# Kernel optimization log

Measured on AMD Instinct MI355X. Metric: run time of the kernel, lower is better.

## Reference

```python
import jax, jax.numpy as jnp
import numpy as np

TOPIC_K = 128
DOC_NUM = 500000
N_ONE = 2048
N_TWO = 64
EPS = 1e-12


def _l2norm(x, axis=-1):
    n = jnp.linalg.norm(x, axis=axis, keepdims=True)
    return x / jnp.maximum(n, EPS)


def _gnn_conv(v_feature, neighbor_mean, Wc, bc, Ws):
    # Conv: linear(neighbor_mean) + self_conv(v_feature) -> relu -> l2 normalize
    h = v_feature @ Ws.T + (neighbor_mean @ Wc.T + bc)
    return _l2norm(jax.nn.relu(h), axis=-1)


def setup_inputs() -> dict:
    key = jax.random.key(0)
    ks = jax.random.split(key, 12)
    K = TOPIC_K
    # Embedding table (xavier-uniform-ish scale)
    lim = float(np.sqrt(6.0 / (DOC_NUM + K)))
    emb = jax.random.uniform(ks[0], (DOC_NUM, K), jnp.float32, -lim, lim)
    s = 1.0 / np.sqrt(K)
    inp = {
        "emb": emb,
        # two_hop_conv params
        "Wc2h": jax.random.uniform(ks[1], (K, K), jnp.float32, -s, s),
        "bc2h": jax.random.uniform(ks[2], (K,), jnp.float32, -s, s),
        "Ws2h": jax.random.uniform(ks[3], (K, K), jnp.float32, -s, s),
        # one_hop_conv params
        "Wc1h": jax.random.uniform(ks[4], (K, K), jnp.float32, -s, s),
        "bc1h": jax.random.uniform(ks[5], (K,), jnp.float32, -s, s),
        "Ws1h": jax.random.uniform(ks[6], (K, K), jnp.float32, -s, s),
        # attention 1x1 single-channel conv weights == scalars
        "w_d": jax.random.normal(ks[7], (), jnp.float32),
        "w_W": jax.random.normal(ks[8], (), jnp.float32),
        "W_mat": jax.random.normal(ks[9], (1, K, K), jnp.float32),
        "v": jax.random.randint(ks[10], (1,), 0, DOC_NUM),
        "one_hop_list": jax.random.randint(ks[11], (N_ONE,), 0, DOC_NUM),
        "two_hop_list": jax.random.randint(jax.random.fold_in(key, 99), (N_ONE, N_TWO), 0, DOC_NUM),
    }
    return inp


def reference(emb, Wc2h, bc2h, Ws2h, Wc1h, bc1h, Ws1h, w_d, w_W, W_mat, v, one_hop_list, two_hop_list):
    # x: embedding of the ego vertex v[0]
    x = emb[v[0]]                                  # [K]
    one_feats = emb[one_hop_list]                  # [n_one, K]
    two_feats = emb[two_hop_list]                  # [n_one, n_two, K]
    # two-hop conv per one-hop neighbor (vectorized over n_one)
    two_mean = two_feats.mean(axis=1)              # [n_one, K]
    one_hop_features = _gnn_conv(one_feats, two_mean, Wc2h, bc2h, Ws2h)  # [n_one, K]
    # one-hop conv for ego vertex
    one_mean = one_hop_features.mean(axis=0)       # [K]
    x = _gnn_conv(x, one_mean, Wc1h, bc1h, Ws1h)   # [K]
    # Attention: 1x1 single-channel convs are scalar multiplies
    d = w_d * x                                    # [K]
    W = w_W * W_mat                                # [1, K, K]
    dW_T = jnp.einsum('k,bjk->bj', d, W)           # matmul(d, W.transpose(1,2)) -> [1, K]
    att = jax.nn.softmax(dW_T[:, None, :] * W_mat, axis=1)  # [1, K, K]
    out = x * att                                  # broadcast over last axis -> [1, K, K]
    # final F.normalize(x) -> l2 normalize along dim=1
    return _l2norm(out, axis=1)
```

## Files before the change

kernel.cpp:

```cpp
#include <hip/hip_runtime.h>
#include <hip/hip_bf16.h>
#include <math.h>

#define K      128
#define NONE   2048
#define NTWO   64
#define NB2    256
#define EPSV   1e-12f
#define PADR   132

#define OFF_TM      0
#define OFF_WT_C2H  (NONE*K)
#define OFF_WT_S2H  (OFF_WT_C2H + K*K)
#define OFF_WT_C1H  (OFF_WT_S2H + K*K)
#define OFF_WT_S1H  (OFF_WT_C1H + K*K)
#define OFF_WT_M    (OFF_WT_S1H + K*K)
#define OFF_P       (OFF_WT_M  + K*K)

__global__ __launch_bounds__(128)
void k1_gather_transpose(const float* __restrict__ emb,
                         const int*   __restrict__ two_hop,
                         const float* __restrict__ Wc2h,
                         const float* __restrict__ Ws2h,
                         const float* __restrict__ Wc1h,
                         const float* __restrict__ Ws1h,
                         const float* __restrict__ Wm,
                         float* __restrict__ ws)
{
    __shared__ int   idxs[NTWO];
    __shared__ __align__(16) float red[4][K];

    const int bid = blockIdx.x;
    const int tid = threadIdx.x;

    if (bid < NONE) {
        if (tid < NTWO) idxs[tid] = two_hop[bid * NTWO + tid];
        __syncthreads();

        const int g  = tid >> 5;
        const int l  = tid & 31;
        const int c0 = l * 4;

        float4 a = make_float4(0.f, 0.f, 0.f, 0.f);
        #pragma unroll
        for (int i = 0; i < 16; ++i) {
            const int n = g + i * 4;
            const float4 e = *(const float4*)&emb[(size_t)idxs[n] * K + c0];
            a.x += e.x; a.y += e.y; a.z += e.z; a.w += e.w;
        }
        *(float4*)&red[g][c0] = a;
        __syncthreads();

        const float sm = red[0][tid] + red[1][tid] + red[2][tid] + red[3][tid];
        ws[OFF_TM + (size_t)bid * K + tid] = sm * (1.f / 64.f);
    } else {
        const int t = bid - NONE;
        const float* src = (t == 0) ? Wc2h : (t == 1) ? Ws2h : (t == 2) ? Wc1h
                         : (t == 3) ? Ws1h : Wm;
        float* dst = ws + ((t == 0) ? OFF_WT_C2H : (t == 1) ? OFF_WT_S2H
                         : (t == 2) ? OFF_WT_C1H : (t == 3) ? OFF_WT_S1H : OFF_WT_M);
        #pragma unroll 4
        for (int k = 0; k < K; ++k)
            dst[k * K + tid] = src[tid * K + k];
    }
}

__global__ __launch_bounds__(512)
void k2_conv2h(const float* __restrict__ emb,
               const int*   __restrict__ one_hop,
               const float* __restrict__ bc2h,
               float* __restrict__ ws)
{
    const int bid  = blockIdx.x;
    const int tid  = threadIdx.x;
    const int w    = tid >> 6;
    const int lane = tid & 63;
    const int h    = lane >> 5;
    const int r    = (lane >> 2) & 7;
    const int qd   = lane & 3;
    const int c0   = w * 16 + qd * 4;
    const int k0   = h * 64;

    __shared__ int onei[8];
    __shared__ __align__(16) float XF[8][PADR];
    __shared__ __align__(16) float MM[8][PADR];
    __shared__ __align__(16) float H [8][PADR];
    __shared__ float SCL[8];

    if (tid < 8) onei[tid] = one_hop[bid * 8 + tid];
    __syncthreads();

    {
        const int sr  = tid >> 5;
        const int pos = (tid & 31) * 4;
        if (sr < 8)
            *(float4*)&XF[sr][pos] =
                *(const float4*)&emb[(size_t)onei[sr] * K + pos];
        else
            *(float4*)&MM[sr - 8][pos] =
                *(const float4*)&ws[OFF_TM + (size_t)(bid * 8 + (sr - 8)) * K + pos];
    }
    __syncthreads();

    const float* WsT = ws + OFF_WT_S2H;
    const float* WcT = ws + OFF_WT_C2H;

    float4 a = make_float4(0.f, 0.f, 0.f, 0.f);
    #pragma unroll 4
    for (int i = 0; i < 64; i += 4) {
        const int k = k0 + i;
        const float4 xv = *(const float4*)&XF[r][k];
        const float4 mv = *(const float4*)&MM[r][k];
        #pragma unroll
        for (int j = 0; j < 4; ++j) {
            const float  xs = (j == 0) ? xv.x : (j == 1) ? xv.y : (j == 2) ? xv.z : xv.w;
            const float  ms = (j == 0) ? mv.x : (j == 1) ? mv.y : (j == 2) ? mv.z : mv.w;
            const float4 sv = *(const float4*)&WsT[(k + j) * K + c0];
            const float4 cv = *(const float4*)&WcT[(k + j) * K + c0];
            a.x += xs * sv.x + ms * cv.x;
            a.y += xs * sv.y + ms * cv.y;
            a.z += xs * sv.z + ms * cv.z;
            a.w += xs * sv.w + ms * cv.w;
        }
    }

    a.x += __shfl_xor(a.x, 32, 64);
    a.y += __shfl_xor(a.y, 32, 64);
    a.z += __shfl_xor(a.z, 32, 64);
    a.w += __shfl_xor(a.w, 32, 64);

    if (h == 0) {
        const float4 bb = *(const float4*)&bc2h[c0];
        H[r][c0 + 0] = fmaxf(a.x + bb.x, 0.f);
        H[r][c0 + 1] = fmaxf(a.y + bb.y, 0.f);
        H[r][c0 + 2] = fmaxf(a.z + bb.z, 0.f);
        H[r][c0 + 3] = fmaxf(a.w + bb.w, 0.f);
    }
    __syncthreads();

    {
        const float h0 = H[w][lane];
        const float h1 = H[w][lane + 64];
        float sq = h0 * h0 + h1 * h1;
        #pragma unroll
        for (int m = 1; m <= 32; m <<= 1) sq += __shfl_xor(sq, m, 64);
        if (lane == 0) SCL[w] = 1.f / fmaxf(sqrtf(sq), EPSV);
    }
    __syncthreads();

    if (tid < K) {
        float s = 0.f;
        #pragma unroll
        for (int rr = 0; rr < 8; ++rr) s += H[rr][tid] * SCL[rr];
        ws[OFF_P + bid * K + tid] = s;
    }
}

__global__ __launch_bounds__(512)
void k3_final(const float* __restrict__ emb,
              const int*   __restrict__ v,
              const float* __restrict__ bc1h,
              const float* __restrict__ w_d,
              const float* __restrict__ w_W,
              const float* __restrict__ Wm,
              const float* __restrict__ ws,
              float* __restrict__ out)
{
    __shared__ float S[K * K];
    __shared__ float X0[K], OM[K], XL[K], DWT[K];
    __shared__ float Q[4][K];
    __shared__ float RED[2];

    const int tid = threadIdx.x;
    const int c   = tid & 127;
    const int q   = tid >> 7;

    const float* P = ws + OFF_P;
    float s = 0.f;
    #pragma unroll 8
    for (int b = q * 64; b < q * 64 + 64; ++b) s += P[b * K + c];
    Q[q][c] = s;
    if (tid < K) X0[tid] = emb[(size_t)v[0] * K + tid];
    __syncthreads();
    if (tid < K)
        OM[tid] = (Q[0][tid] + Q[1][tid] + Q[2][tid] + Q[3][tid]) * (1.f / 2048.f);
    __syncthreads();

    const float* WsT1 = ws + OFF_WT_S1H;
    const float* WcT1 = ws + OFF_WT_C1H;
    float acc = 0.f;
    #pragma unroll 4
    for (int k = q * 32; k < q * 32 + 32; ++k)
        acc += X0[k] * WsT1[k * K + c] + OM[k] * WcT1[k * K + c];
    Q[q][c] = acc;
    __syncthreads();

    float r_ = 0.f;
    if (tid < K) {
        const float a = Q[0][tid] + Q[1][tid] + Q[2][tid] + Q[3][tid] + bc1h[tid];
        r_ = fmaxf(a, 0.f);
        float sq = r_ * r_;
        #pragma unroll
        for (int m = 1; m <= 32; m <<= 1) sq += __shfl_xor(sq, m, 64);
        if ((tid & 63) == 0) RED[tid >> 6] = sq;
    }
    __syncthreads();
    if (tid < K) {
        const float tot = RED[0] + RED[1];
        XL[tid] = r_ / fmaxf(sqrtf(tot), EPSV);
    }
    __syncthreads();

    const float* WmT = ws + OFF_WT_M;
    float a2 = 0.f;
    #pragma unroll 4
    for (int k = q * 32; k < q * 32 + 32; ++k)
        a2 += XL[k] * WmT[k * K + c];
    Q[q][c] = a2;
    __syncthreads();
    if (tid < K)
        DWT[tid] = w_d[0] * w_W[0] * (Q[0][tid] + Q[1][tid] + Q[2][tid] + Q[3][tid]);
    __syncthreads();

    const float dk = DWT[c];
    const float xv = XL[c];
    const int   j0 = q * 32;

    float mx = -INFINITY;
    #pragma unroll 4
    for (int j = j0; j < j0 + 32; ++j) {
        const float sv = dk * Wm[j * K + c];
        S[j * K + c] = sv;
        mx = fmaxf(mx, sv);
    }
    Q[q][c] = mx;
    __syncthreads();
    const float M = fmaxf(fmaxf(Q[0][c], Q[1][c]), fmaxf(Q[2][c], Q[3][c]));
    __syncthreads();

    float sm = 0.f;
    #pragma unroll 4
    for (int j = j0; j < j0 + 32; ++j) {
        const float e = expf(S[j * K + c] - M);
        S[j * K + c] = e;
        sm += e;
    }
    Q[q][c] = sm;
    __syncthreads();
    const float SUM = Q[0][c] + Q[1][c] + Q[2][c] + Q[3][c];
    const float inv = xv / SUM;
    __syncthreads();

    float s2 = 0.f;
    #pragma unroll 4
    for (int j = j0; j < j0 + 32; ++j) {
        const float o = S[j * K + c] * inv;
        s2 += o * o;
    }
    Q[q][c] = s2;
    __syncthreads();
    const float scn =
        1.f / fmaxf(sqrtf(Q[0][c] + Q[1][c] + Q[2][c] + Q[3][c]), EPSV);

    #pragma unroll 4
    for (int j = j0; j < j0 + 32; ++j)
        out[j * K + c] = S[j * K + c] * inv * scn;
}

extern "C" void kernel_launch(void* const* d_in, const int* in_sizes, int n_in,
                              void* d_out, int out_size, void* d_ws, size_t ws_size,
                              hipStream_t stream)
{
    const float* emb     = (const float*)d_in[0];
    const float* Wc2h    = (const float*)d_in[1];
    const float* bc2h    = (const float*)d_in[2];
    const float* Ws2h    = (const float*)d_in[3];
    const float* Wc1h    = (const float*)d_in[4];
    const float* bc1h    = (const float*)d_in[5];
    const float* Ws1h    = (const float*)d_in[6];
    const float* w_d     = (const float*)d_in[7];
    const float* w_W     = (const float*)d_in[8];
    const float* Wm      = (const float*)d_in[9];
    const int*   v       = (const int*)d_in[10];
    const int*   one_hop = (const int*)d_in[11];
    const int*   two_hop = (const int*)d_in[12];
    float*       out     = (float*)d_out;
    float*       ws      = (float*)d_ws;

    hipLaunchKernelGGL(k1_gather_transpose, dim3(NONE + 5), dim3(128), 0, stream,
                       emb, two_hop, Wc2h, Ws2h, Wc1h, Ws1h, Wm, ws);
    hipLaunchKernelGGL(k2_conv2h, dim3(NB2), dim3(512), 0, stream,
                       emb, one_hop, bc2h, ws);
    hipLaunchKernelGGL(k3_final, dim3(1), dim3(512), 0, stream,
                       emb, v, bc1h, w_d, w_W, Wm, ws, out);
}
```

Measured before the change: 364.0 us.

## Fuse two-hop gather into conv kernel and drop weight-transpose pre-pass

Merges the two-hop neighbor gather/mean kernel into the conv kernel, so each 512-thread block gathers its own 8 rows' neighbor means directly into shared memory instead of writing and rereading a workspace buffer. The 2-hop weights are transposed on the fly into shared-memory tiles per 16-wide k chunk, and the final kernel reads the untransposed 1-hop and attention weights row-wise with float4 loads. This removes one launch and the global round trip for the means and transposed weights. In exchange, the gather now runs on only 256 blocks, which exposes less memory-level parallelism for the random embedding reads, and each block repeats the weight tiling.

```diff
diff --git a/kernel.cpp b/kernel.cpp
--- a/kernel.cpp
+++ b/kernel.cpp
@@ -5,69 +5,17 @@
 #define K      128
 #define NONE   2048
 #define NTWO   64
-#define NB2    256
+#define NB     256
 #define EPSV   1e-12f
 #define PADR   132
 
-#define OFF_TM      0
-#define OFF_WT_C2H  (NONE*K)
-#define OFF_WT_S2H  (OFF_WT_C2H + K*K)
-#define OFF_WT_C1H  (OFF_WT_S2H + K*K)
-#define OFF_WT_S1H  (OFF_WT_C1H + K*K)
-#define OFF_WT_M    (OFF_WT_S1H + K*K)
-#define OFF_P       (OFF_WT_M  + K*K)
-
-__global__ __launch_bounds__(128)
-void k1_gather_transpose(const float* __restrict__ emb,
-                         const int*   __restrict__ two_hop,
-                         const float* __restrict__ Wc2h,
-                         const float* __restrict__ Ws2h,
-                         const float* __restrict__ Wc1h,
-                         const float* __restrict__ Ws1h,
-                         const float* __restrict__ Wm,
-                         float* __restrict__ ws)
-{
-    __shared__ int   idxs[NTWO];
-    __shared__ __align__(16) float red[4][K];
-
-    const int bid = blockIdx.x;
-    const int tid = threadIdx.x;
-
-    if (bid < NONE) {
-        if (tid < NTWO) idxs[tid] = two_hop[bid * NTWO + tid];
-        __syncthreads();
-
-        const int g  = tid >> 5;
-        const int l  = tid & 31;
-        const int c0 = l * 4;
-
-        float4 a = make_float4(0.f, 0.f, 0.f, 0.f);
-        #pragma unroll
-        for (int i = 0; i < 16; ++i) {
-            const int n = g + i * 4;
-            const float4 e = *(const float4*)&emb[(size_t)idxs[n] * K + c0];
-            a.x += e.x; a.y += e.y; a.z += e.z; a.w += e.w;
-        }
-        *(float4*)&red[g][c0] = a;
-        __syncthreads();
-
-        const float sm = red[0][tid] + red[1][tid] + red[2][tid] + red[3][tid];
-        ws[OFF_TM + (size_t)bid * K + tid] = sm * (1.f / 64.f);
-    } else {
-        const int t = bid - NONE;
-        const float* src = (t == 0) ? Wc2h : (t == 1) ? Ws2h : (t == 2) ? Wc1h
-                         : (t == 3) ? Ws1h : Wm;
-        float* dst = ws + ((t == 0) ? OFF_WT_C2H : (t == 1) ? OFF_WT_S2H
-                         : (t == 2) ? OFF_WT_C1H : (t == 3) ? OFF_WT_S1H : OFF_WT_M);
-        #pragma unroll 4
-        for (int k = 0; k < K; ++k)
-            dst[k * K + tid] = src[tid * K + k];
-    }
-}
 
 __global__ __launch_bounds__(512)
-void k2_conv2h(const float* __restrict__ emb,
+void k12_fused(const float* __restrict__ emb,
                const int*   __restrict__ one_hop,
+               const int*   __restrict__ two_hop,
+               const float* __restrict__ Ws2h,
+               const float* __restrict__ Wc2h,
                const float* __restrict__ bc2h,
                float* __restrict__ ws)
 {
@@ -75,66 +23,103 @@
     const int tid  = threadIdx.x;
     const int w    = tid >> 6;
     const int lane = tid & 63;
-    const int h    = lane >> 5;
-    const int r    = (lane >> 2) & 7;
-    const int qd   = lane & 3;
-    const int c0   = w * 16 + qd * 4;
-    const int k0   = h * 64;
-
-    __shared__ int onei[8];
+
+    __shared__ int SIDX[8][NTWO];
     __shared__ __align__(16) float XF[8][PADR];
     __shared__ __align__(16) float MM[8][PADR];
     __shared__ __align__(16) float H [8][PADR];
+    __shared__ __align__(16) float SW[16][PADR];
+    __shared__ __align__(16) float CW[16][PADR];
     __shared__ float SCL[8];
 
-    if (tid < 8) onei[tid] = one_hop[bid * 8 + tid];
-    __syncthreads();
-
-    {
-        const int sr  = tid >> 5;
-        const int pos = (tid & 31) * 4;
-        if (sr < 8)
-            *(float4*)&XF[sr][pos] =
-                *(const float4*)&emb[(size_t)onei[sr] * K + pos];
-        else
-            *(float4*)&MM[sr - 8][pos] =
-                *(const float4*)&ws[OFF_TM + (size_t)(bid * 8 + (sr - 8)) * K + pos];
-    }
-    __syncthreads();
-
-    const float* WsT = ws + OFF_WT_S2H;
-    const float* WcT = ws + OFF_WT_C2H;
+    const int R = bid * 8 + w;
+
+    SIDX[w][lane] = two_hop[R * NTWO + lane];
+
+    const int g  = lane >> 5;
+    const int c0 = (lane & 31) * 4;
+
+    const int oneIdx = one_hop[R];
+    float4 ego = make_float4(0.f, 0.f, 0.f, 0.f);
+    if (g == 0)
+        ego = *(const float4*)&emb[(size_t)oneIdx * K + c0];
+
+    __syncthreads();
 
     float4 a = make_float4(0.f, 0.f, 0.f, 0.f);
-    #pragma unroll 4
-    for (int i = 0; i < 64; i += 4) {
-        const int k = k0 + i;
-        const float4 xv = *(const float4*)&XF[r][k];
-        const float4 mv = *(const float4*)&MM[r][k];
-        #pragma unroll
-        for (int j = 0; j < 4; ++j) {
-            const float  xs = (j == 0) ? xv.x : (j == 1) ? xv.y : (j == 2) ? xv.z : xv.w;
-            const float  ms = (j == 0) ? mv.x : (j == 1) ? mv.y : (j == 2) ? mv.z : mv.w;
-            const float4 sv = *(const float4*)&WsT[(k + j) * K + c0];
-            const float4 cv = *(const float4*)&WcT[(k + j) * K + c0];
-            a.x += xs * sv.x + ms * cv.x;
-            a.y += xs * sv.y + ms * cv.y;
-            a.z += xs * sv.z + ms * cv.z;
-            a.w += xs * sv.w + ms * cv.w;
-        }
-    }
-
+    #pragma unroll
+    for (int i = 0; i < 32; ++i) {
+        const int row = SIDX[w][g + 2 * i];
+        const float4 e = *(const float4*)&emb[(size_t)row * K + c0];
+        a.x += e.x; a.y += e.y; a.z += e.z; a.w += e.w;
+    }
     a.x += __shfl_xor(a.x, 32, 64);
     a.y += __shfl_xor(a.y, 32, 64);
     a.z += __shfl_xor(a.z, 32, 64);
     a.w += __shfl_xor(a.w, 32, 64);
 
+    if (g == 0) {
+        *(float4*)&XF[w][c0] = ego;
+        const float inv64 = 1.f / 64.f;
+        MM[w][c0 + 0] = a.x * inv64;
+        MM[w][c0 + 1] = a.y * inv64;
+        MM[w][c0 + 2] = a.z * inv64;
+        MM[w][c0 + 3] = a.w * inv64;
+    }
+    __syncthreads();
+
+    const int h  = lane >> 5;
+    const int r  = (lane >> 2) & 7;
+    const int qd = lane & 3;
+    const int cc = w * 16 + qd * 4;
+
+    const int sc = tid >> 2;
+    const int q4 = tid & 3;
+
+    float4 acc = make_float4(0.f, 0.f, 0.f, 0.f);
+
+    for (int t = 0; t < 8; ++t) {
+        {
+            const float4 sv = *(const float4*)&Ws2h[(size_t)sc * K + t * 16 + q4 * 4];
+            const float4 cv = *(const float4*)&Wc2h[(size_t)sc * K + t * 16 + q4 * 4];
+            SW[q4 * 4 + 0][sc] = sv.x; SW[q4 * 4 + 1][sc] = sv.y;
+            SW[q4 * 4 + 2][sc] = sv.z; SW[q4 * 4 + 3][sc] = sv.w;
+            CW[q4 * 4 + 0][sc] = cv.x; CW[q4 * 4 + 1][sc] = cv.y;
+            CW[q4 * 4 + 2][sc] = cv.z; CW[q4 * 4 + 3][sc] = cv.w;
+        }
+        __syncthreads();
+
+        #pragma unroll
+        for (int j2 = 0; j2 < 2; ++j2) {
+            const int kb = h * 8 + j2 * 4;
+            const float4 xv = *(const float4*)&XF[r][t * 16 + kb];
+            const float4 mv = *(const float4*)&MM[r][t * 16 + kb];
+            #pragma unroll
+            for (int jj = 0; jj < 4; ++jj) {
+                const float xs = (jj == 0) ? xv.x : (jj == 1) ? xv.y : (jj == 2) ? xv.z : xv.w;
+                const float ms = (jj == 0) ? mv.x : (jj == 1) ? mv.y : (jj == 2) ? mv.z : mv.w;
+                const float4 sv = *(const float4*)&SW[kb + jj][cc];
+                const float4 cv = *(const float4*)&CW[kb + jj][cc];
+                acc.x += xs * sv.x + ms * cv.x;
+                acc.y += xs * sv.y + ms * cv.y;
+                acc.z += xs * sv.z + ms * cv.z;
+                acc.w += xs * sv.w + ms * cv.w;
+            }
+        }
+        __syncthreads();
+    }
+
+    acc.x += __shfl_xor(acc.x, 32, 64);
+    acc.y += __shfl_xor(acc.y, 32, 64);
+    acc.z += __shfl_xor(acc.z, 32, 64);
+    acc.w += __shfl_xor(acc.w, 32, 64);
+
     if (h == 0) {
-        const float4 bb = *(const float4*)&bc2h[c0];
-        H[r][c0 + 0] = fmaxf(a.x + bb.x, 0.f);
-        H[r][c0 + 1] = fmaxf(a.y + bb.y, 0.f);
-        H[r][c0 + 2] = fmaxf(a.z + bb.z, 0.f);
-        H[r][c0 + 3] = fmaxf(a.w + bb.w, 0.f);
+        const float4 bb = *(const float4*)&bc2h[cc];
+        H[r][cc + 0] = fmaxf(acc.x + bb.x, 0.f);
+        H[r][cc + 1] = fmaxf(acc.y + bb.y, 0.f);
+        H[r][cc + 2] = fmaxf(acc.z + bb.z, 0.f);
+        H[r][cc + 3] = fmaxf(acc.w + bb.w, 0.f);
     }
     __syncthreads();
 
@@ -152,13 +137,15 @@
         float s = 0.f;
         #pragma unroll
         for (int rr = 0; rr < 8; ++rr) s += H[rr][tid] * SCL[rr];
-        ws[OFF_P + bid * K + tid] = s;
+        ws[bid * K + tid] = s;
     }
 }
 
 __global__ __launch_bounds__(512)
 void k3_final(const float* __restrict__ emb,
               const int*   __restrict__ v,
+              const float* __restrict__ Ws1h,
+              const float* __restrict__ Wc1h,
               const float* __restrict__ bc1h,
               const float* __restrict__ w_d,
               const float* __restrict__ w_W,
@@ -175,7 +162,7 @@
     const int c   = tid & 127;
     const int q   = tid >> 7;
 
-    const float* P = ws + OFF_P;
+    const float* P = ws;
     float s = 0.f;
     #pragma unroll 8
     for (int b = q * 64; b < q * 64 + 64; ++b) s += P[b * K + c];
@@ -186,13 +173,20 @@
         OM[tid] = (Q[0][tid] + Q[1][tid] + Q[2][tid] + Q[3][tid]) * (1.f / 2048.f);
     __syncthreads();
 
-    const float* WsT1 = ws + OFF_WT_S1H;
-    const float* WcT1 = ws + OFF_WT_C1H;
-    float acc = 0.f;
-    #pragma unroll 4
-    for (int k = q * 32; k < q * 32 + 32; ++k)
-        acc += X0[k] * WsT1[k * K + c] + OM[k] * WcT1[k * K + c];
-    Q[q][c] = acc;
+    {
+        const float* Wsr = Ws1h + (size_t)c * K + q * 32;
+        const float* Wcr = Wc1h + (size_t)c * K + q * 32;
+        float acc = 0.f;
+        #pragma unroll
+        for (int kk = 0; kk < 32; kk += 4) {
+            const float4 sv = *(const float4*)&Wsr[kk];
+            const float4 cv = *(const float4*)&Wcr[kk];
+            const int k = q * 32 + kk;
+            acc += X0[k+0]*sv.x + X0[k+1]*sv.y + X0[k+2]*sv.z + X0[k+3]*sv.w
+                 + OM[k+0]*cv.x + OM[k+1]*cv.y + OM[k+2]*cv.z + OM[k+3]*cv.w;
+        }
+        Q[q][c] = acc;
+    }
     __syncthreads();
 
     float r_ = 0.f;
@@ -211,12 +205,17 @@
     }
     __syncthreads();
 
-    const float* WmT = ws + OFF_WT_M;
-    float a2 = 0.f;
-    #pragma unroll 4
-    for (int k = q * 32; k < q * 32 + 32; ++k)
-        a2 += XL[k] * WmT[k * K + c];
-    Q[q][c] = a2;
+    {
+        const float* Wmr = Wm + (size_t)c * K + q * 32;
+        float a2 = 0.f;
+        #pragma unroll
+        for (int kk = 0; kk < 32; kk += 4) {
+            const float4 wv = *(const float4*)&Wmr[kk];
+            const int k = q * 32 + kk;
+            a2 += XL[k+0]*wv.x + XL[k+1]*wv.y + XL[k+2]*wv.z + XL[k+3]*wv.w;
+        }
+        Q[q][c] = a2;
+    }
     __syncthreads();
     if (tid < K)
         DWT[tid] = w_d[0] * w_W[0] * (Q[0][tid] + Q[1][tid] + Q[2][tid] + Q[3][tid]);
@@ -287,10 +286,8 @@
     float*       out     = (float*)d_out;
     float*       ws      = (float*)d_ws;
 
-    hipLaunchKernelGGL(k1_gather_transpose, dim3(NONE + 5), dim3(128), 0, stream,
-                       emb, two_hop, Wc2h, Ws2h, Wc1h, Ws1h, Wm, ws);
-    hipLaunchKernelGGL(k2_conv2h, dim3(NB2), dim3(512), 0, stream,
-                       emb, one_hop, bc2h, ws);
+    hipLaunchKernelGGL(k12_fused, dim3(NB), dim3(512), 0, stream,
+                       emb, one_hop, two_hop, Ws2h, Wc2h, bc2h, ws);
     hipLaunchKernelGGL(k3_final, dim3(1), dim3(512), 0, stream,
-                       emb, v, bc1h, w_d, w_W, Wm, ws, out);
+                       emb, v, Ws1h, Wc1h, bc1h, w_d, w_W, Wm, ws, out);
 }
```

After: 343.5 us. 5.6% less time.
